# Kernel optimization log

Hardware: AMD Instinct MI355X
Metric: run time of the kernel (lower is better)

Reference implementation:

```python
import jax, jax.numpy as jnp
import numpy as np


def _quantize(x, weight):
    # x: (B, D, H, W); weight: (D, K)
    B, D, H, W = x.shape
    K = weight.shape[1]
    xf = x.reshape(B, D, H * W)  # (B, D, N)
    x2 = jnp.sum(xf * xf, axis=1)                      # (B, N)
    cross = jnp.einsum('bdn,dk->bnk', xf, weight)       # (B, N, K)
    e2 = jnp.sum(weight * weight, axis=0)               # (K,)
    d2 = x2[..., None] - 2.0 * cross + e2               # (B, N, K)
    argmin = jnp.argmin(d2, axis=-1)                    # (B, N)
    # gather codes: (B, N, D) -> (B, D, N) -> (B, D, H, W)
    quant = weight.T[argmin]                            # (B, N, D)
    result = jnp.transpose(quant, (0, 2, 1)).reshape(B, D, H, W)
    return result, argmin.reshape(B, H, W)


def setup_inputs() -> dict:
    key = jax.random.key(0)
    k1, k2 = jax.random.split(key)
    x = jax.random.normal(k1, (32, 256, 32, 32), dtype=jnp.float32)
    weight = jax.random.uniform(k2, (256, 512), dtype=jnp.float32)  # torch.rand init
    return {"x": x, "weight": weight}


def reference(x, weight):
    result, argmin = _quantize(x, weight)
    return result, argmin
```

## Files before the change

kernel.cpp:

```cpp
#include <hip/hip_runtime.h>

typedef __attribute__((ext_vector_type(8))) short bf16x8;
typedef __attribute__((ext_vector_type(16))) float f32x16;

__device__ __forceinline__ bool lex_lt(float av, int ai, float bv, int bi) {
  return av < bv || (av == bv && ai < bi);
}

__device__ __forceinline__ unsigned bf16_rne(float v) {
  unsigned u = __float_as_uint(v);
  return (u + 0x7fffu + ((u >> 16) & 1u)) >> 16;
}

__device__ __forceinline__ unsigned pk_bf16(float a, float b) {
  return bf16_rne(a) | (bf16_rne(b) << 16);
}

__global__ __launch_bounds__(256) void vq_pre(
    const float* __restrict__ w, float* __restrict__ e2,
    short* __restrict__ wtil, float* __restrict__ wT) {
  int blk = blockIdx.x;
  if (blk < 64) {
    int gid = blk * 256 + threadIdx.x;
    int n  = gid & 511;
    int kg = gid >> 9;
    bf16x8 hv, lv;
    float vv[8];
#pragma unroll
    for (int j = 0; j < 8; ++j) {
      float v = w[(kg * 8 + j) * 512 + n];
      vv[j] = v;
      unsigned h = bf16_rne(v);
      float hf = __uint_as_float(h << 16);
      unsigned l = bf16_rne(v - hf);
      hv[j] = (short)h;
      lv[j] = (short)l;
    }
    short* dst = wtil + (size_t)gid * 8;
    *(bf16x8*)dst = hv;
    *(bf16x8*)(dst + 131072) = lv;
    if (wT) {
      float* p = wT + (size_t)n * 256 + kg * 8;
      *(float4*)p       = make_float4(vv[0], vv[1], vv[2], vv[3]);
      *(float4*)(p + 4) = make_float4(vv[4], vv[5], vv[6], vv[7]);
    }
  } else {
    int t = (blk - 64) * 256 + threadIdx.x;
    int k = t >> 2;
    int part = t & 3;
    double s = 0.0;
#pragma unroll 8
    for (int d = part * 64; d < part * 64 + 64; ++d) {
      double v = (double)w[d * 512 + k];
      s = fma(v, v, s);
    }
    s += __shfl_xor(s, 1);
    s += __shfl_xor(s, 2);
    if (part == 0) e2[k] = (float)s;
  }
}

__global__ __launch_bounds__(512, 2) void vq_main(
    const float* __restrict__ x, const float* __restrict__ w,
    const float* __restrict__ e2g, const short* __restrict__ wtil,
    const float* __restrict__ wT,
    float* __restrict__ out, float* __restrict__ arg_out) {
  __shared__ __align__(16) char arena[151552];
  short* xh   = (short*)arena;
  short* xl   = (short*)(arena + 65536);
  float* e2s  = (float*)(arena + 131072);
  float* tv1  = (float*)(arena + 133120);
  float* tv2  = (float*)(arena + 137216);
  int*   ti1  = (int*)(arena + 141312);
  int*   ti2  = (int*)(arena + 145408);
  int*   p1S  = (int*)(arena + 149504);
  int*   p2S  = (int*)(arena + 150016);
  int*   needS= (int*)(arena + 150528);
  int*   rpickS=(int*)(arena + 151040);
  float* gbuf = (float*)arena;

  const int tid = threadIdx.x;
  const int b  = blockIdx.x >> 3;
  const int n0 = (blockIdx.x & 7) << 7;
  const float* xbase = x + (size_t)b * 262144 + n0;

  {
    const int n4  = tid & 31;
    const int kgp = tid >> 5;
#pragma unroll
    for (int rep = 0; rep < 2; ++rep) {
      int kg = kgp + (rep << 4);
      float4 v[8];
#pragma unroll
      for (int j = 0; j < 8; ++j)
        v[j] = *(const float4*)(xbase + (size_t)(kg * 8 + j) * 1024 + (n4 << 2));
#pragma unroll
      for (int i = 0; i < 4; ++i) {
        int m = (n4 << 2) + i;
        union { int w4[4]; bf16x8 v8; } H, L;
#pragma unroll
        for (int jj = 0; jj < 4; ++jj) {
          float a = (i == 0) ? v[2*jj].x : (i == 1) ? v[2*jj].y : (i == 2) ? v[2*jj].z : v[2*jj].w;
          float c = (i == 0) ? v[2*jj+1].x : (i == 1) ? v[2*jj+1].y : (i == 2) ? v[2*jj+1].z : v[2*jj+1].w;
          unsigned hu = pk_bf16(a, c);
          float haf = __uint_as_float(hu << 16);
          float hcf = __uint_as_float(hu & 0xffff0000u);
          unsigned lu = pk_bf16(a - haf, c - hcf);
          H.w4[jj] = (int)hu;
          L.w4[jj] = (int)lu;
        }
        int off = (m << 8) + ((kg ^ (m & 7)) << 3);
        *(bf16x8*)&xh[off] = H.v8;
        *(bf16x8*)&xl[off] = L.v8;
      }
    }
    e2s[tid] = e2g[tid];
  }
  __syncthreads();

  const int lane = tid & 63;
  const int wv   = tid >> 6;
  const int ln   = lane & 31;
  const int half = lane >> 5;
  const int wb   = wv << 6;

  f32x16 acc[2][4];
#pragma unroll
  for (int ct = 0; ct < 2; ++ct)
#pragma unroll
    for (int pt = 0; pt < 4; ++pt)
#pragma unroll
      for (int r = 0; r < 16; ++r) acc[ct][pt][r] = 0.f;

  const int asw = ln & 7;
  const int abase = ln << 8;

  int bofs[2];
#pragma unroll
  for (int ct = 0; ct < 2; ++ct) bofs[ct] = (wb + (ct << 5) + ln) << 3;

  bf16x8 pch[2], pcl[2];
#pragma unroll
  for (int ct = 0; ct < 2; ++ct) {
    const short* p = wtil + (half << 12) + bofs[ct];
    pch[ct] = *(const bf16x8*)p;
    pcl[ct] = *(const bf16x8*)(p + 131072);
  }

#pragma unroll
  for (int ch = 0; ch < 16; ++ch) {
    const int kg = (ch << 1) + half;
    const int ao = abase + ((kg ^ asw) << 3);
    bf16x8 xf[4], xg[4];
#pragma unroll
    for (int pt = 0; pt < 4; ++pt) {
      xf[pt] = *(const bf16x8*)&xh[ao + (pt << 13)];
      xg[pt] = *(const bf16x8*)&xl[ao + (pt << 13)];
    }
    bf16x8 cfh[2], cfl[2];
#pragma unroll
    for (int ct = 0; ct < 2; ++ct) { cfh[ct] = pch[ct]; cfl[ct] = pcl[ct]; }
    if (ch < 15) {
      const int kgn = ((ch + 1) << 1) + half;
#pragma unroll
      for (int ct = 0; ct < 2; ++ct) {
        const short* p = wtil + (kgn << 12) + bofs[ct];
        pch[ct] = *(const bf16x8*)p;
        pcl[ct] = *(const bf16x8*)(p + 131072);
      }
    }
#pragma unroll
    for (int ct = 0; ct < 2; ++ct)
#pragma unroll
      for (int pt = 0; pt < 4; ++pt) {
        acc[ct][pt] = __builtin_amdgcn_mfma_f32_32x32x16_bf16(cfh[ct], xf[pt], acc[ct][pt], 0, 0, 0);
        acc[ct][pt] = __builtin_amdgcn_mfma_f32_32x32x16_bf16(cfh[ct], xg[pt], acc[ct][pt], 0, 0, 0);
        acc[ct][pt] = __builtin_amdgcn_mfma_f32_32x32x16_bf16(cfl[ct], xf[pt], acc[ct][pt], 0, 0, 0);
      }
  }

  float e2r[2][16];
#pragma unroll
  for (int ct = 0; ct < 2; ++ct)
#pragma unroll
    for (int r = 0; r < 16; ++r)
      e2r[ct][r] = e2s[wb + (ct << 5) + (r & 3) + ((r >> 2) << 3) + (half << 2)];

#pragma unroll
  for (int pt = 0; pt < 4; ++pt) {
    float v1 = 3.4e38f, v2 = 3.4e38f;
    int i1 = 0x7fffffff, i2 = 0x7fffffff;
#pragma unroll
    for (int ct = 0; ct < 2; ++ct) {
#pragma unroll
      for (int r = 0; r < 16; ++r) {
        int k = wb + (ct << 5) + (r & 3) + ((r >> 2) << 3) + (half << 2);
        float s = fmaf(-2.f, acc[ct][pt][r], e2r[ct][r]);
        if (lex_lt(s, k, v1, i1)) { v2 = v1; i2 = i1; v1 = s; i1 = k; }
        else if (lex_lt(s, k, v2, i2)) { v2 = s; i2 = k; }
      }
    }
    {
      float ov1 = __shfl_xor(v1, 32);
      int   oi1 = __shfl_xor(i1, 32);
      float ov2 = __shfl_xor(v2, 32);
      int   oi2 = __shfl_xor(i2, 32);
      bool aFirst = lex_lt(v1, i1, ov1, oi1);
      float nv1 = aFirst ? v1 : ov1;  int ni1 = aFirst ? i1 : oi1;
      float cv  = aFirst ? ov1 : v1;  int ci  = aFirst ? oi1 : i1;
      float sv  = aFirst ? v2 : ov2;  int si  = aFirst ? i2 : oi2;
      bool cFirst = lex_lt(cv, ci, sv, si);
      v1 = nv1; i1 = ni1;
      v2 = cFirst ? cv : sv; i2 = cFirst ? ci : si;
    }
    if (half == 0) {
      int s = (wv << 7) + (pt << 5) + ln;
      tv1[s] = v1; ti1[s] = i1; tv2[s] = v2; ti2[s] = i2;
    }
  }
  __syncthreads();

  if (tid < 128) {
    int row = tid;
    float v1 = 3.4e38f, v2 = 3.4e38f;
    int i1 = 0x7fffffff, i2 = 0x7fffffff;
#pragma unroll
    for (int wvv = 0; wvv < 8; ++wvv) {
      int s = (wvv << 7) + row;
      float a1 = tv1[s]; int ai = ti1[s];
      float a2 = tv2[s]; int bi = ti2[s];
      if (lex_lt(a1, ai, v1, i1)) { v2 = v1; i2 = i1; v1 = a1; i1 = ai; }
      else if (lex_lt(a1, ai, v2, i2)) { v2 = a1; i2 = ai; }
      if (lex_lt(a2, bi, v1, i1)) { v2 = v1; i2 = i1; v1 = a2; i1 = bi; }
      else if (lex_lt(a2, bi, v2, i2)) { v2 = a2; i2 = bi; }
    }
    p1S[row] = i1; p2S[row] = i2;
    needS[row] = (v2 - v1 < 0.01f) ? 1 : 0;
    rpickS[row] = i1;
  }
  __syncthreads();

  for (int t = 0; t < 16; ++t) {
    int row = (t << 3) + wv;
    if (needS[row]) {
      int i1 = p1S[row], i2 = p2S[row];
      const float* xp = x + (size_t)b * 262144 + n0 + row;
      double s1 = 0.0, s2 = 0.0;
      int k0 = lane << 2;
#pragma unroll
      for (int i = 0; i < 4; ++i) {
        int k = k0 + i;
        double xv = (double)xp[(size_t)k * 1024];
        double w1 = (double)w[k * 512 + i1];
        double w2 = (double)w[k * 512 + i2];
        double t1 = xv - w1, t2 = xv - w2;
        s1 = fma(t1, t1, s1);
        s2 = fma(t2, t2, s2);
      }
#pragma unroll
      for (int off = 32; off >= 1; off >>= 1) {
        s1 += __shfl_xor(s1, off);
        s2 += __shfl_xor(s2, off);
      }
      if (lane == 0 && (s2 < s1 || (s2 == s1 && i2 < i1))) rpickS[row] = i2;
    }
  }
  __syncthreads();

  if (tid < 128) arg_out[b * 1024 + n0 + tid] = (float)rpickS[tid];

  if (wT) {
    {
      const int pos  = tid >> 2;
      const int dseg = tid & 3;
      const float* wrow = wT + (size_t)rpickS[pos] * 256;
#pragma unroll
      for (int j = 0; j < 16; ++j) {
        int d = (j << 4) + (dseg << 2);
        float4 v = *(const float4*)(wrow + d);
        int base = pos * 265 + d + (d >> 5);
        gbuf[base]     = v.x;
        gbuf[base + 1] = v.y;
        gbuf[base + 2] = v.z;
        gbuf[base + 3] = v.w;
      }
    }
    __syncthreads();
    {
      const int nn0 = (tid & 31) << 2;
      const int d0g = tid >> 5;
      float* obase = out + (size_t)b * 262144 + n0 + nn0;
#pragma unroll
      for (int dg = 0; dg < 16; ++dg) {
        int d = d0g + (dg << 4);
        int sa = d + (d >> 5);
        float4 o;
        o.x = gbuf[(nn0 + 0) * 265 + sa];
        o.y = gbuf[(nn0 + 1) * 265 + sa];
        o.z = gbuf[(nn0 + 2) * 265 + sa];
        o.w = gbuf[(nn0 + 3) * 265 + sa];
        *(float4*)(obase + (size_t)d * 1024) = o;
      }
    }
  } else {
    const int nn0 = (tid & 31) << 2;
    const int d0g = tid >> 5;
    int pk0 = rpickS[nn0], pk1 = rpickS[nn0 + 1], pk2 = rpickS[nn0 + 2], pk3 = rpickS[nn0 + 3];
    float* obase = out + (size_t)b * 262144 + n0 + nn0;
#pragma unroll
    for (int dg = 0; dg < 16; ++dg) {
      int d = d0g + (dg << 4);
      const float* wr = w + d * 512;
      float4 o = make_float4(wr[pk0], wr[pk1], wr[pk2], wr[pk3]);
      *(float4*)(obase + (size_t)d * 1024) = o;
    }
  }
}

extern "C" void kernel_launch(void* const* d_in, const int* in_sizes, int n_in,
                              void* d_out, int out_size, void* d_ws, size_t ws_size,
                              hipStream_t stream) {
  const float* x = (const float*)d_in[0];
  const float* w = (const float*)d_in[1];
  float* out  = (float*)d_out;
  float* argf = out + 8388608;
  float* e2   = (float*)d_ws;
  short* wtil = (short*)((char*)d_ws + 2048);
  size_t need = 2048 + 524288 + 524288;
  float* wT   = (ws_size >= need) ? (float*)((char*)d_ws + 2048 + 524288) : nullptr;

  vq_pre<<<72, 256, 0, stream>>>(w, e2, wtil, wT);
  vq_main<<<256, 512, 0, stream>>>(x, w, e2, wtil, wT, out, argf);
}
```

Before: 124.1 us.

## Overlap second half of x staging with MFMA k-steps and transpose gather buffer

```diff
diff --git a/kernel.cpp b/kernel.cpp
--- a/kernel.cpp
+++ b/kernel.cpp
@@ -84,36 +84,40 @@
   const int n0 = (blockIdx.x & 7) << 7;
   const float* xbase = x + (size_t)b * 262144 + n0;
 
+  const int n4  = tid & 31;
+  const int kgp = tid >> 5;
+
+  auto load8 = [&](int kg, float4* v) {
+#pragma unroll
+    for (int j = 0; j < 8; ++j)
+      v[j] = *(const float4*)(xbase + (size_t)(kg * 8 + j) * 1024 + (n4 << 2));
+  };
+  auto convert_write = [&](int kg, const float4* v) {
+#pragma unroll
+    for (int i = 0; i < 4; ++i) {
+      int m = (n4 << 2) + i;
+      union { int w4[4]; bf16x8 v8; } H, L;
+#pragma unroll
+      for (int jj = 0; jj < 4; ++jj) {
+        float a = (i == 0) ? v[2*jj].x : (i == 1) ? v[2*jj].y : (i == 2) ? v[2*jj].z : v[2*jj].w;
+        float c = (i == 0) ? v[2*jj+1].x : (i == 1) ? v[2*jj+1].y : (i == 2) ? v[2*jj+1].z : v[2*jj+1].w;
+        unsigned hu = pk_bf16(a, c);
+        float haf = __uint_as_float(hu << 16);
+        float hcf = __uint_as_float(hu & 0xffff0000u);
+        unsigned lu = pk_bf16(a - haf, c - hcf);
+        H.w4[jj] = (int)hu;
+        L.w4[jj] = (int)lu;
+      }
+      int off = (m << 8) + ((kg ^ (m & 7)) << 3);
+      *(bf16x8*)&xh[off] = H.v8;
+      *(bf16x8*)&xl[off] = L.v8;
+    }
+  };
+
   {
-    const int n4  = tid & 31;
-    const int kgp = tid >> 5;
-#pragma unroll
-    for (int rep = 0; rep < 2; ++rep) {
-      int kg = kgp + (rep << 4);
-      float4 v[8];
-#pragma unroll
-      for (int j = 0; j < 8; ++j)
-        v[j] = *(const float4*)(xbase + (size_t)(kg * 8 + j) * 1024 + (n4 << 2));
-#pragma unroll
-      for (int i = 0; i < 4; ++i) {
-        int m = (n4 << 2) + i;
-        union { int w4[4]; bf16x8 v8; } H, L;
-#pragma unroll
-        for (int jj = 0; jj < 4; ++jj) {
-          float a = (i == 0) ? v[2*jj].x : (i == 1) ? v[2*jj].y : (i == 2) ? v[2*jj].z : v[2*jj].w;
-          float c = (i == 0) ? v[2*jj+1].x : (i == 1) ? v[2*jj+1].y : (i == 2) ? v[2*jj+1].z : v[2*jj+1].w;
-          unsigned hu = pk_bf16(a, c);
-          float haf = __uint_as_float(hu << 16);
-          float hcf = __uint_as_float(hu & 0xffff0000u);
-          unsigned lu = pk_bf16(a - haf, c - hcf);
-          H.w4[jj] = (int)hu;
-          L.w4[jj] = (int)lu;
-        }
-        int off = (m << 8) + ((kg ^ (m & 7)) << 3);
-        *(bf16x8*)&xh[off] = H.v8;
-        *(bf16x8*)&xl[off] = L.v8;
-      }
-    }
+    float4 v0[8];
+    load8(kgp, v0);
+    convert_write(kgp, v0);
     e2s[tid] = e2g[tid];
   }
   __syncthreads();
@@ -147,8 +151,7 @@
     pcl[ct] = *(const bf16x8*)(p + 131072);
   }
 
-#pragma unroll
-  for (int ch = 0; ch < 16; ++ch) {
+  auto kstep = [&](int ch) {
     const int kg = (ch << 1) + half;
     const int ao = abase + ((kg ^ asw) << 3);
     bf16x8 xf[4], xg[4];
@@ -177,7 +180,16 @@
         acc[ct][pt] = __builtin_amdgcn_mfma_f32_32x32x16_bf16(cfh[ct], xg[pt], acc[ct][pt], 0, 0, 0);
         acc[ct][pt] = __builtin_amdgcn_mfma_f32_32x32x16_bf16(cfl[ct], xf[pt], acc[ct][pt], 0, 0, 0);
       }
-  }
+  };
+
+  float4 vx[8];
+  load8(kgp + 16, vx);
+  kstep(0); kstep(1); kstep(2); kstep(3);
+  convert_write(kgp + 16, vx);
+  kstep(4); kstep(5); kstep(6); kstep(7);
+  __syncthreads();
+  kstep(8); kstep(9); kstep(10); kstep(11);
+  kstep(12); kstep(13); kstep(14); kstep(15);
 
   float e2r[2][16];
 #pragma unroll
@@ -276,13 +288,12 @@
       const float* wrow = wT + (size_t)rpickS[pos] * 256;
 #pragma unroll
       for (int j = 0; j < 16; ++j) {
-        int d = (j << 4) + (dseg << 2);
-        float4 v = *(const float4*)(wrow + d);
-        int base = pos * 265 + d + (d >> 5);
-        gbuf[base]     = v.x;
-        gbuf[base + 1] = v.y;
-        gbuf[base + 2] = v.z;
-        gbuf[base + 3] = v.w;
+        int d0 = (j << 4) + (dseg << 2);
+        float4 v = *(const float4*)(wrow + d0);
+        gbuf[(d0 + 0) * 132 + pos] = v.x;
+        gbuf[(d0 + 1) * 132 + pos] = v.y;
+        gbuf[(d0 + 2) * 132 + pos] = v.z;
+        gbuf[(d0 + 3) * 132 + pos] = v.w;
       }
     }
     __syncthreads();
@@ -293,12 +304,7 @@
 #pragma unroll
       for (int dg = 0; dg < 16; ++dg) {
         int d = d0g + (dg << 4);
-        int sa = d + (d >> 5);
-        float4 o;
-        o.x = gbuf[(nn0 + 0) * 265 + sa];
-        o.y = gbuf[(nn0 + 1) * 265 + sa];
-        o.z = gbuf[(nn0 + 2) * 265 + sa];
-        o.w = gbuf[(nn0 + 3) * 265 + sa];
+        float4 o = *(const float4*)&gbuf[d * 132 + nn0];
         *(float4*)(obase + (size_t)d * 1024) = o;
       }
     }
```

New measurement: 120.1 us. 1.03x faster.
